# Kernel tuning notes

Hardware: AMD Instinct MI355X
Metric: run time of the kernel (lower is better)

## Reference

```python
import jax, jax.numpy as jnp
import numpy as np

B, T, C_IN, H, W = 128, 12, 10, 25, 25
HID = 64
DN = ('NCHW', 'OIHW', 'NCHW')


def setup_inputs() -> dict:
    key = jax.random.key(0)
    ks = jax.random.split(key, 8)
    x = jax.random.normal(ks[0], (B, T, C_IN, H, W), dtype=jnp.float32)
    # ConvLSTM cell: conv over concat([x, h]) -> 4*HID gate channels, 3x3 kernel
    conv_w = jax.random.normal(ks[1], (4 * HID, C_IN + HID, 3, 3), dtype=jnp.float32) * 0.05
    conv_b = jnp.zeros((4 * HID,), dtype=jnp.float32)
    # MLP head: hidden*25*25 -> 16 -> 8 -> 2
    w1 = jax.random.normal(ks[2], (HID * H * W, 16), dtype=jnp.float32) * 0.01
    b1 = jnp.zeros((16,), dtype=jnp.float32)
    w2 = jax.random.normal(ks[3], (16, 8), dtype=jnp.float32) * 0.1
    b2 = jnp.zeros((8,), dtype=jnp.float32)
    w3 = jax.random.normal(ks[4], (8, 2), dtype=jnp.float32) * 0.1
    b3 = jnp.zeros((2,), dtype=jnp.float32)
    return {"x": x, "conv_w": conv_w, "conv_b": conv_b,
            "w1": w1, "b1": b1, "w2": w2, "b2": b2, "w3": w3, "b3": b3}


def _convlstm_last_h(x, conv_w, conv_b):
    # x: (B,T,C,H,W); returns last hidden state h_T: (B,HID,H,W)
    h0 = jnp.zeros((x.shape[0], HID, H, W), dtype=x.dtype)
    c0 = jnp.zeros_like(h0)

    def step(carry, xt):
        h, c = carry
        inp = jnp.concatenate([xt, h], axis=1)              # (B, C+HID, H, W)
        gates = jax.lax.conv_general_dilated(
            inp, conv_w, window_strides=(1, 1), padding='SAME',
            dimension_numbers=DN) + conv_b[None, :, None, None]  # (B,4*HID,H,W)
        i, f, o, g = jnp.split(gates, 4, axis=1)
        i, f, o = jax.nn.sigmoid(i), jax.nn.sigmoid(f), jax.nn.sigmoid(o)
        g = jnp.tanh(g)
        c_new = f * c + i * g
        h_new = o * jnp.tanh(c_new)
        return (h_new, c_new), None

    (h_last, _), _ = jax.lax.scan(step, (h0, c0), jnp.swapaxes(x, 0, 1))
    return h_last


def reference(x, conv_w, conv_b, w1, b1, w2, b2, w3, b3):
    h = _convlstm_last_h(x, conv_w, conv_b)          # (B,HID,25,25)
    h = jax.nn.relu(h).reshape(h.shape[0], -1)       # flatten
    # dropout is identity in eval mode
    h = jax.nn.relu(h @ w1 + b1)
    h = jax.nn.relu(h @ w2 + b2)
    logits = h @ w3 + b3                             # (B,2)
    return jax.nn.log_softmax(logits, axis=1)
```

## Files before the change

kernel.cpp:

```cpp
#include <hip/hip_runtime.h>
#include <hip/hip_bf16.h>
#include <math.h>

#define BATCH 128
#define TT    12
#define CIN   10
#define HID   64
#define PLANE 625
#define NU    10
#define IPB   50000
#define NKB   45
#define CSZ   (BATCH*PLANE*HID)
#define KSPLIT 10

typedef __attribute__((ext_vector_type(8)))  short bf16x8;
typedef __attribute__((ext_vector_type(16))) float f32x16;

__device__ __forceinline__ float fsigm(float v){ return 1.f/(1.f+__expf(-v)); }
__device__ __forceinline__ float ftanh(float v){ return 1.f - 2.f/(__expf(2.f*v)+1.f); }
__device__ __forceinline__ unsigned short f2bf(float v){
    __hip_bfloat16 b = __float2bfloat16(v);
    return *reinterpret_cast<unsigned short*>(&b);
}

__global__ void k_wprep(const float* __restrict__ w, unsigned short* __restrict__ wpk){
    int tid = blockIdx.x*256 + threadIdx.x;
    if (tid >= NKB*8*64) return;
    int lane = tid & 63;
    int nt   = (tid >> 6) & 7;
    int kb   = tid >> 9;
    int tap = kb/5, ci = kb - tap*5;
    int ky = tap/3, kx = tap - ky*3;
    int g = lane & 3, jlo = (lane & 31) >> 2, kh = lane >> 5;
    int o = g*64 + nt*8 + jlo;
    union { unsigned short u[8]; float4 f; } pk;
    #pragma unroll
    for (int e = 0; e < 8; ++e){
        int ch = ci*16 + kh*8 + e;
        float v = (ch < 74) ? w[((o*74 + ch)*3 + ky)*3 + kx] : 0.f;
        pk.u[e] = f2bf(v);
    }
    *reinterpret_cast<float4*>(wpk + (size_t)tid*8) = pk.f;
}

__global__ void k_w1prep(const float* __restrict__ w1, float* __restrict__ w1t){
    int tid = blockIdx.x*256 + threadIdx.x;
    if (tid >= 40000*4) return;
    int rowp = tid >> 2, f4 = tid & 3;
    int m = rowp >> 6, j = rowp & 63;
    const float4* src = (const float4*)(w1 + (size_t)(j*625 + m)*16);
    ((float4*)(w1t + (size_t)rowp*16))[f4] = src[f4];
}

__global__ void k_xcopy(const float* __restrict__ x, unsigned short* __restrict__ inp, int t){
    int idx = blockIdx.x*256 + threadIdx.x;
    if (idx >= BATCH*CIN*PLANE) return;
    int m  = idx % PLANE;
    int r  = idx / PLANE;
    int ch = r % CIN;
    int b  = r / CIN;
    float v = x[((size_t)(b*TT + t)*CIN + ch)*PLANE + m];
    inp[(size_t)b*IPB + ((((ch>>3)*PLANE) + m)<<3) + (ch&7)] = f2bf(v);
}

__global__ __launch_bounds__(512) void k_gemm(
    const float* __restrict__ x,
    const unsigned short* __restrict__ inp,
    unsigned short* __restrict__ inpn,
    const unsigned short* __restrict__ wpk,
    const float* __restrict__ bias,
    float* __restrict__ cbuf,
    unsigned short* __restrict__ hbf,
    int t)
{
    __shared__ __align__(16) unsigned short at2[1620*8];

    const int tid  = threadIdx.x;
    const int mg   = blockIdx.x;
    const int b    = blockIdx.y;
    const int lane = tid & 63;
    const int nt   = tid >> 6;
    const int rlo  = (mg*64)/25;

    const unsigned short* ib = inp + (size_t)b*IPB;
    for (int idx = tid; idx < 1620; idx += 512){
        int q   = idx/162, pix = idx - q*162;
        int rr  = pix/27,  cc  = pix - rr*27;
        int gr  = rlo - 1 + rr, gc = cc - 1;
        float4 v = {0.f,0.f,0.f,0.f};
        if ((unsigned)gr < 25u && (unsigned)gc < 25u)
            v = *reinterpret_cast<const float4*>(ib + (((size_t)q*PLANE + gr*25 + gc)<<3));
        *reinterpret_cast<float4*>(at2 + ((size_t)idx<<3)) = v;
    }

    const int kh = lane >> 5;
    const unsigned short* ap[2];
    #pragma unroll
    for (int mt = 0; mt < 2; ++mt){
        int m = mg*64 + mt*32 + (lane & 31);
        int row = m/25, col = m - row*25;
        int pm = (row - rlo + 1)*27 + col;
        ap[mt] = at2 + kh*1296 + ((pm - 27) << 3);
    }

    f32x16 acc[2];
    #pragma unroll
    for (int mt = 0; mt < 2; ++mt)
        #pragma unroll
        for (int e = 0; e < 16; ++e) acc[mt][e] = 0.f;

    __syncthreads();

    const bf16x8* wptr = reinterpret_cast<const bf16x8*>(wpk) + nt*64 + lane;
    bf16x8 bcur = *wptr;
    const unsigned short *a0 = ap[0], *a1 = ap[1];
    #pragma unroll 1
    for (int tap = 0; tap < 9; ++tap){
        #pragma unroll
        for (int ci = 0; ci < 5; ++ci){
            bf16x8 bnxt = wptr[512];
            wptr += 512;
            bf16x8 f0 = *reinterpret_cast<const bf16x8*>(a0 + ci*2592);
            bf16x8 f1 = *reinterpret_cast<const bf16x8*>(a1 + ci*2592);
            acc[0] = __builtin_amdgcn_mfma_f32_32x32x16_bf16(f0, bcur, acc[0], 0,0,0);
            acc[1] = __builtin_amdgcn_mfma_f32_32x32x16_bf16(f1, bcur, acc[1], 0,0,0);
            bcur = bnxt;
        }
        const int d = (tap == 2 || tap == 5) ? 25*8 : 8;
        a0 += d; a1 += d;
    }

    const int g   = lane & 3;
    const int jlo = (lane & 31) >> 2;
    const int j   = nt*8 + jlo;
    const float bown = bias[g*64 + j];
    const float sA = (g == 3) ? 2.f : 1.f;
    const float sB = (g == 3) ? -1.f : 0.f;
    const int  mbase = mg*64 + 4*kh;
    const bool gb0 = (g & 1), gb1 = (g & 2);
    float* cb = cbuf + (size_t)b*PLANE*HID;
    unsigned short* hn  = inpn + (size_t)b*IPB;
    unsigned short* hfb = hbf  + (size_t)b*40000;
    const int chh = CIN + j, uh = chh >> 3, sh = chh & 7;

    #pragma unroll
    for (int mt = 0; mt < 2; ++mt){
        #pragma unroll
        for (int rq = 0; rq < 4; ++rq){
            float v0 = fmaf(sA, fsigm(sA*(acc[mt][rq*4+0] + bown)), sB);
            float v1 = fmaf(sA, fsigm(sA*(acc[mt][rq*4+1] + bown)), sB);
            float v2 = fmaf(sA, fsigm(sA*(acc[mt][rq*4+2] + bown)), sB);
            float v3 = fmaf(sA, fsigm(sA*(acc[mt][rq*4+3] + bown)), sB);
            float s;
            s = __shfl_xor(gb0 ? v0 : v1, 1); if (gb0) v0 = s; else v1 = s;
            s = __shfl_xor(gb0 ? v2 : v3, 1); if (gb0) v2 = s; else v3 = s;
            s = __shfl_xor(gb1 ? v0 : v2, 2); if (gb1) v0 = s; else v2 = s;
            s = __shfl_xor(gb1 ? v1 : v3, 2); if (gb1) v1 = s; else v3 = s;
            const int m = mbase + mt*32 + g + 8*rq;
            if (m < PLANE){
                float co = cb[m*HID + j];
                float cn = fmaf(v1, co, v0*v3);
                float h  = v2 * ftanh(cn);
                if (t < TT-1){
                    cb[m*HID + j] = cn;
                    hn[((uh*PLANE + m) << 3) + sh] = f2bf(h);
                } else {
                    hfb[m*64 + j] = f2bf(h > 0.f ? h : 0.f);
                }
            }
        }
    }

    if (t < TT-1){
        const float* xn = x + (size_t)(b*TT + t + 1)*CIN*PLANE;
        for (int idx = tid; idx < 640; idx += 512){
            int ch = idx >> 6, mi = idx & 63;
            int m = mg*64 + mi;
            if (m < PLANE)
                inpn[(size_t)b*IPB + ((((ch>>3)*PLANE) + m)<<3) + (ch&7)] =
                    f2bf(xn[ch*PLANE + m]);
        }
    }
}

__global__ __launch_bounds__(256) void k_mlp1(
    const unsigned short* __restrict__ hbf, const float* __restrict__ w1t,
    float* __restrict__ part)
{
    __shared__ float xw[4][4][16];
    const int ks = blockIdx.x, bg = blockIdx.y, tid = threadIdx.x;
    const int kw0 = ks*4000, kw1 = kw0 + 4000;
    const unsigned short* h0 = hbf + (size_t)(bg*4+0)*40000;
    const unsigned short* h1 = hbf + (size_t)(bg*4+1)*40000;
    const unsigned short* h2 = hbf + (size_t)(bg*4+2)*40000;
    const unsigned short* h3 = hbf + (size_t)(bg*4+3)*40000;

    float acc[4][16];
    #pragma unroll
    for (int bi = 0; bi < 4; ++bi)
        #pragma unroll
        for (int n = 0; n < 16; ++n) acc[bi][n] = 0.f;

    for (int kw = kw0 + tid*2; kw < kw1; kw += 512){
        const float4* wp = (const float4*)(w1t + (size_t)kw*16);
        float4 q0 = wp[0], q1 = wp[1], q2 = wp[2], q3 = wp[3];
        float4 r0 = wp[4], r1 = wp[5], r2 = wp[6], r3 = wp[7];
        unsigned int u0 = *(const unsigned int*)(h0 + kw);
        unsigned int u1 = *(const unsigned int*)(h1 + kw);
        unsigned int u2 = *(const unsigned int*)(h2 + kw);
        unsigned int u3 = *(const unsigned int*)(h3 + kw);
        #define ACC1(bi, u) { \
            float fl = __uint_as_float((u) << 16); \
            float fh = __uint_as_float((u) & 0xffff0000u); \
            acc[bi][ 0]=fmaf(fl,q0.x,fmaf(fh,r0.x,acc[bi][ 0])); \
            acc[bi][ 1]=fmaf(fl,q0.y,fmaf(fh,r0.y,acc[bi][ 1])); \
            acc[bi][ 2]=fmaf(fl,q0.z,fmaf(fh,r0.z,acc[bi][ 2])); \
            acc[bi][ 3]=fmaf(fl,q0.w,fmaf(fh,r0.w,acc[bi][ 3])); \
            acc[bi][ 4]=fmaf(fl,q1.x,fmaf(fh,r1.x,acc[bi][ 4])); \
            acc[bi][ 5]=fmaf(fl,q1.y,fmaf(fh,r1.y,acc[bi][ 5])); \
            acc[bi][ 6]=fmaf(fl,q1.z,fmaf(fh,r1.z,acc[bi][ 6])); \
            acc[bi][ 7]=fmaf(fl,q1.w,fmaf(fh,r1.w,acc[bi][ 7])); \
            acc[bi][ 8]=fmaf(fl,q2.x,fmaf(fh,r2.x,acc[bi][ 8])); \
            acc[bi][ 9]=fmaf(fl,q2.y,fmaf(fh,r2.y,acc[bi][ 9])); \
            acc[bi][10]=fmaf(fl,q2.z,fmaf(fh,r2.z,acc[bi][10])); \
            acc[bi][11]=fmaf(fl,q2.w,fmaf(fh,r2.w,acc[bi][11])); \
            acc[bi][12]=fmaf(fl,q3.x,fmaf(fh,r3.x,acc[bi][12])); \
            acc[bi][13]=fmaf(fl,q3.y,fmaf(fh,r3.y,acc[bi][13])); \
            acc[bi][14]=fmaf(fl,q3.z,fmaf(fh,r3.z,acc[bi][14])); \
            acc[bi][15]=fmaf(fl,q3.w,fmaf(fh,r3.w,acc[bi][15])); }
        ACC1(0, u0) ACC1(1, u1) ACC1(2, u2) ACC1(3, u3)
        #undef ACC1
    }

    #pragma unroll
    for (int d = 1; d < 64; d <<= 1)
        #pragma unroll
        for (int bi = 0; bi < 4; ++bi)
            #pragma unroll
            for (int n = 0; n < 16; ++n) acc[bi][n] += __shfl_xor(acc[bi][n], d);
    if ((tid & 63) == 0){
        int w = tid >> 6;
        #pragma unroll
        for (int bi = 0; bi < 4; ++bi)
            #pragma unroll
            for (int n = 0; n < 16; ++n) xw[w][bi][n] = acc[bi][n];
    }
    __syncthreads();
    if (tid < 64){
        int bi = tid >> 4, n = tid & 15;
        float s = xw[0][bi][n] + xw[1][bi][n] + xw[2][bi][n] + xw[3][bi][n];
        part[((size_t)(bg*4 + bi)*KSPLIT + ks)*16 + n] = s;
    }
}

__global__ __launch_bounds__(128) void k_mlp2(
    const float* __restrict__ part,
    const float* __restrict__ b1,
    const float* __restrict__ w2, const float* __restrict__ b2,
    const float* __restrict__ w3, const float* __restrict__ b3,
    float* __restrict__ out)
{
    const int b = threadIdx.x;
    float h1[16];
    #pragma unroll
    for (int i = 0; i < 16; ++i) h1[i] = b1[i];
    for (int s = 0; s < KSPLIT; ++s)
        #pragma unroll
        for (int i = 0; i < 16; ++i) h1[i] += part[((size_t)b * KSPLIT + s) * 16 + i];
    #pragma unroll
    for (int i = 0; i < 16; ++i) h1[i] = h1[i] > 0.f ? h1[i] : 0.f;

    float h2[8];
    #pragma unroll
    for (int i = 0; i < 8; ++i){
        float s2 = b2[i];
        #pragma unroll
        for (int k2 = 0; k2 < 16; ++k2) s2 += h1[k2] * w2[k2*8 + i];
        h2[i] = s2 > 0.f ? s2 : 0.f;
    }
    float l0 = b3[0], l1 = b3[1];
    #pragma unroll
    for (int k3 = 0; k3 < 8; ++k3){ l0 += h2[k3]*w3[k3*2]; l1 += h2[k3]*w3[k3*2+1]; }
    float m   = fmaxf(l0, l1);
    float lse = m + logf(__expf(l0 - m) + __expf(l1 - m));
    out[b*2 + 0] = l0 - lse;
    out[b*2 + 1] = l1 - lse;
}

extern "C" void kernel_launch(void* const* d_in, const int* in_sizes, int n_in,
                              void* d_out, int out_size, void* d_ws, size_t ws_size,
                              hipStream_t stream) {
    const float* x      = (const float*)d_in[0];
    const float* conv_w = (const float*)d_in[1];
    const float* conv_b = (const float*)d_in[2];
    const float* w1     = (const float*)d_in[3];
    const float* b1     = (const float*)d_in[4];
    const float* w2     = (const float*)d_in[5];
    const float* b2     = (const float*)d_in[6];
    const float* w3     = (const float*)d_in[7];
    const float* b3     = (const float*)d_in[8];
    float* out = (float*)d_out;

    unsigned short* inp0 = (unsigned short*)d_ws;
    unsigned short* inp1 = inp0 + (size_t)BATCH*IPB;
    float* c   = (float*)(inp1 + (size_t)BATCH*IPB);
    unsigned short* hbf = (unsigned short*)(c + CSZ);
    unsigned short* wpk = hbf + (size_t)BATCH*40000;
    float* w1t  = (float*)(wpk + (size_t)(NKB+1)*8*64*8);
    float* part = w1t + 640000;

    hipMemsetAsync(inp0, 0, (size_t)BATCH*IPB*2, stream);
    hipMemsetAsync(inp1, 0, (size_t)BATCH*IPB*2, stream);
    hipMemsetAsync(c,    0, (size_t)CSZ*4,       stream);

    k_wprep <<<dim3(90),   dim3(256), 0, stream>>>(conv_w, wpk);
    k_w1prep<<<dim3(625),  dim3(256), 0, stream>>>(w1, w1t);
    k_xcopy <<<dim3(3125), dim3(256), 0, stream>>>(x, inp0, 0);

    for (int t = 0; t < TT; ++t){
        unsigned short* ic  = (t & 1) ? inp1 : inp0;
        unsigned short* in_ = (t & 1) ? inp0 : inp1;
        k_gemm<<<dim3(10, BATCH), dim3(512), 0, stream>>>(x, ic, in_, wpk, conv_b, c, hbf, t);
    }
    k_mlp1<<<dim3(KSPLIT, 32), dim3(256), 0, stream>>>(hbf, w1t, part);
    k_mlp2<<<dim3(1), dim3(128), 0, stream>>>(part, b1, w2, b2, w3, b3, out);
}
```

Measured before the change: 625.0 us.

## Double M tile per block and stage conv weights into LDS via async loads

Result: slower. 711.4 us (+13.8%).

```diff
diff --git a/kernel.cpp b/kernel.cpp
--- a/kernel.cpp
+++ b/kernel.cpp
@@ -10,6 +10,7 @@
 #define NU    10
 #define IPB   50000
 #define NKB   45
+#define NKB_ALLOC (NKB+6)
 #define CSZ   (BATCH*PLANE*HID)
 #define KSPLIT 10
 
@@ -63,6 +64,9 @@
     inp[(size_t)b*IPB + ((((ch>>3)*PLANE) + m)<<3) + (ch&7)] = f2bf(v);
 }
 
+__device__ constexpr int TOFF[9] = {0,8,16,216,224,232,432,440,448};
+#define AOFF(kb) (TOFF[(kb)/5] + ((kb)%5)*3456)
+
 __global__ __launch_bounds__(512) void k_gemm(
     const float* __restrict__ x,
     const unsigned short* __restrict__ inp,
@@ -73,20 +77,23 @@
     unsigned short* __restrict__ hbf,
     int t)
 {
-    __shared__ __align__(16) unsigned short at2[1620*8];
+    __shared__ __align__(16) unsigned short at2[2160*8];
+    __shared__ __align__(16) unsigned short wls[2][8192];
 
     const int tid  = threadIdx.x;
     const int mg   = blockIdx.x;
     const int b    = blockIdx.y;
     const int lane = tid & 63;
-    const int nt   = tid >> 6;
-    const int rlo  = (mg*64)/25;
+    const int w    = tid >> 6;
+    const int ntp  = w & 3;
+    const int mtp  = w >> 2;
+    const int r0row = (mg*128)/25;
 
     const unsigned short* ib = inp + (size_t)b*IPB;
-    for (int idx = tid; idx < 1620; idx += 512){
-        int q   = idx/162, pix = idx - q*162;
+    for (int idx = tid; idx < 2160; idx += 512){
+        int q   = idx/216, pix = idx - q*216;
         int rr  = pix/27,  cc  = pix - rr*27;
-        int gr  = rlo - 1 + rr, gc = cc - 1;
+        int gr  = r0row - 1 + rr, gc = cc - 1;
         float4 v = {0.f,0.f,0.f,0.f};
         if ((unsigned)gr < 25u && (unsigned)gc < 25u)
             v = *reinterpret_cast<const float4*>(ib + (((size_t)q*PLANE + gr*25 + gc)<<3));
@@ -94,78 +101,101 @@
     }
 
     const int kh = lane >> 5;
-    const unsigned short* ap[2];
-    #pragma unroll
-    for (int mt = 0; mt < 2; ++mt){
-        int m = mg*64 + mt*32 + (lane & 31);
-        int row = m/25, col = m - row*25;
-        int pm = (row - rlo + 1)*27 + col;
-        ap[mt] = at2 + kh*1296 + ((pm - 27) << 3);
-    }
-
-    f32x16 acc[2];
-    #pragma unroll
-    for (int mt = 0; mt < 2; ++mt)
-        #pragma unroll
-        for (int e = 0; e < 16; ++e) acc[mt][e] = 0.f;
-
-    __syncthreads();
-
-    const bf16x8* wptr = reinterpret_cast<const bf16x8*>(wpk) + nt*64 + lane;
-    bf16x8 bcur = *wptr;
-    const unsigned short *a0 = ap[0], *a1 = ap[1];
-    #pragma unroll 1
-    for (int tap = 0; tap < 9; ++tap){
-        #pragma unroll
-        for (int ci = 0; ci < 5; ++ci){
-            bf16x8 bnxt = wptr[512];
-            wptr += 512;
-            bf16x8 f0 = *reinterpret_cast<const bf16x8*>(a0 + ci*2592);
-            bf16x8 f1 = *reinterpret_cast<const bf16x8*>(a1 + ci*2592);
-            acc[0] = __builtin_amdgcn_mfma_f32_32x32x16_bf16(f0, bcur, acc[0], 0,0,0);
-            acc[1] = __builtin_amdgcn_mfma_f32_32x32x16_bf16(f1, bcur, acc[1], 0,0,0);
-            bcur = bnxt;
+    const unsigned short *a0, *a1;
+    {
+        int m0 = mg*128 + (mtp*2+0)*32 + (lane & 31);
+        int r_ = m0/25, c_ = m0 - r_*25;
+        a0 = at2 + kh*1728 + (((r_ - r0row + 1)*27 + c_ - 27) << 3);
+        int m1 = mg*128 + (mtp*2+1)*32 + (lane & 31);
+        r_ = m1/25; c_ = m1 - r_*25;
+        a1 = at2 + kh*1728 + (((r_ - r0row + 1)*27 + c_ - 27) << 3);
+    }
+    const unsigned short* bb = &wls[0][0] + ntp*1024 + lane*8;
+
+    auto stageB = [&](int kb, int bufsel, int slot){
+        __builtin_amdgcn_global_load_lds(
+            (const __attribute__((address_space(1))) void*)(wpk + ((size_t)(kb*8 + w))*512 + lane*8),
+            (__attribute__((address_space(3))) void*)(&wls[bufsel][slot*4096 + w*512]),
+            16, 0, 0);
+    };
+
+    f32x16 acc00, acc01, acc10, acc11;
+    #pragma unroll
+    for (int e = 0; e < 16; ++e){ acc00[e]=0.f; acc01[e]=0.f; acc10[e]=0.f; acc11[e]=0.f; }
+
+    stageB(0, 0, 0);
+    stageB(1, 0, 1);
+
+    #define KBSTEP(kb, buf, q) { \
+        bf16x8 b0 = *reinterpret_cast<const bf16x8*>(bb + (buf)*8192 + (q)*4096); \
+        bf16x8 b1 = *reinterpret_cast<const bf16x8*>(bb + (buf)*8192 + (q)*4096 + 512); \
+        bf16x8 f0 = *reinterpret_cast<const bf16x8*>(a0 + AOFF(kb)); \
+        bf16x8 f1 = *reinterpret_cast<const bf16x8*>(a1 + AOFF(kb)); \
+        acc00 = __builtin_amdgcn_mfma_f32_32x32x16_bf16(f0, b0, acc00, 0,0,0); \
+        acc10 = __builtin_amdgcn_mfma_f32_32x32x16_bf16(f1, b0, acc10, 0,0,0); \
+        acc01 = __builtin_amdgcn_mfma_f32_32x32x16_bf16(f0, b1, acc01, 0,0,0); \
+        acc11 = __builtin_amdgcn_mfma_f32_32x32x16_bf16(f1, b1, acc11, 0,0,0); \
+    }
+
+    #pragma unroll
+    for (int p = 0; p < 23; ++p){
+        __syncthreads();
+        if (p < 21){
+            stageB(2*p+2, (p+1)&1, 0);
+            stageB(2*p+3, (p+1)&1, 1);
+        } else if (p == 21){
+            stageB(44, 0, 0);
         }
-        const int d = (tap == 2 || tap == 5) ? 25*8 : 8;
-        a0 += d; a1 += d;
-    }
+        KBSTEP(2*p, p&1, 0);
+        if (2*p+1 < NKB) KBSTEP(2*p+1, p&1, 1);
+    }
+    #undef KBSTEP
 
     const int g   = lane & 3;
     const int jlo = (lane & 31) >> 2;
-    const int j   = nt*8 + jlo;
-    const float bown = bias[g*64 + j];
+    const int j0  = (ntp*2+0)*8 + jlo;
+    const int j1  = (ntp*2+1)*8 + jlo;
+    const float bown0 = bias[g*64 + j0];
+    const float bown1 = bias[g*64 + j1];
     const float sA = (g == 3) ? 2.f : 1.f;
     const float sB = (g == 3) ? -1.f : 0.f;
-    const int  mbase = mg*64 + 4*kh;
+    const int  mbase = mg*128 + mtp*64 + 4*kh;
     const bool gb0 = (g & 1), gb1 = (g & 2);
     float* cb = cbuf + (size_t)b*PLANE*HID;
     unsigned short* hn  = inpn + (size_t)b*IPB;
     unsigned short* hfb = hbf  + (size_t)b*40000;
-    const int chh = CIN + j, uh = chh >> 3, sh = chh & 7;
-
-    #pragma unroll
-    for (int mt = 0; mt < 2; ++mt){
-        #pragma unroll
-        for (int rq = 0; rq < 4; ++rq){
-            float v0 = fmaf(sA, fsigm(sA*(acc[mt][rq*4+0] + bown)), sB);
-            float v1 = fmaf(sA, fsigm(sA*(acc[mt][rq*4+1] + bown)), sB);
-            float v2 = fmaf(sA, fsigm(sA*(acc[mt][rq*4+2] + bown)), sB);
-            float v3 = fmaf(sA, fsigm(sA*(acc[mt][rq*4+3] + bown)), sB);
-            float s;
-            s = __shfl_xor(gb0 ? v0 : v1, 1); if (gb0) v0 = s; else v1 = s;
-            s = __shfl_xor(gb0 ? v2 : v3, 1); if (gb0) v2 = s; else v3 = s;
-            s = __shfl_xor(gb1 ? v0 : v2, 2); if (gb1) v0 = s; else v2 = s;
-            s = __shfl_xor(gb1 ? v1 : v3, 2); if (gb1) v1 = s; else v3 = s;
-            const int m = mbase + mt*32 + g + 8*rq;
-            if (m < PLANE){
-                float co = cb[m*HID + j];
-                float cn = fmaf(v1, co, v0*v3);
-                float h  = v2 * ftanh(cn);
-                if (t < TT-1){
-                    cb[m*HID + j] = cn;
-                    hn[((uh*PLANE + m) << 3) + sh] = f2bf(h);
-                } else {
-                    hfb[m*64 + j] = f2bf(h > 0.f ? h : 0.f);
+
+    #pragma unroll
+    for (int mt_ = 0; mt_ < 2; ++mt_){
+        #pragma unroll
+        for (int n = 0; n < 2; ++n){
+            const f32x16& A = (mt_ == 0) ? (n == 0 ? acc00 : acc01)
+                                         : (n == 0 ? acc10 : acc11);
+            const int   jj = n ? j1 : j0;
+            const float bw = n ? bown1 : bown0;
+            const int  chh = CIN + jj, uh = chh >> 3, sh = chh & 7;
+            #pragma unroll
+            for (int rq = 0; rq < 4; ++rq){
+                float v0 = fmaf(sA, fsigm(sA*(A[rq*4+0] + bw)), sB);
+                float v1 = fmaf(sA, fsigm(sA*(A[rq*4+1] + bw)), sB);
+                float v2 = fmaf(sA, fsigm(sA*(A[rq*4+2] + bw)), sB);
+                float v3 = fmaf(sA, fsigm(sA*(A[rq*4+3] + bw)), sB);
+                float s;
+                s = __shfl_xor(gb0 ? v0 : v1, 1); if (gb0) v0 = s; else v1 = s;
+                s = __shfl_xor(gb0 ? v2 : v3, 1); if (gb0) v2 = s; else v3 = s;
+                s = __shfl_xor(gb1 ? v0 : v2, 2); if (gb1) v0 = s; else v2 = s;
+                s = __shfl_xor(gb1 ? v1 : v3, 2); if (gb1) v1 = s; else v3 = s;
+                const int m = mbase + mt_*32 + g + 8*rq;
+                if (m < PLANE){
+                    float co = cb[m*HID + jj];
+                    float cn = fmaf(v1, co, v0*v3);
+                    float h  = v2 * ftanh(cn);
+                    if (t < TT-1){
+                        cb[m*HID + jj] = cn;
+                        hn[((uh*PLANE + m) << 3) + sh] = f2bf(h);
+                    } else {
+                        hfb[m*64 + jj] = f2bf(h > 0.f ? h : 0.f);
+                    }
                 }
             }
         }
@@ -173,9 +203,9 @@
 
     if (t < TT-1){
         const float* xn = x + (size_t)(b*TT + t + 1)*CIN*PLANE;
-        for (int idx = tid; idx < 640; idx += 512){
-            int ch = idx >> 6, mi = idx & 63;
-            int m = mg*64 + mi;
+        for (int idx = tid; idx < 1280; idx += 512){
+            int ch = idx >> 7, mi = idx & 127;
+            int m = mg*128 + mi;
             if (m < PLANE)
                 inpn[(size_t)b*IPB + ((((ch>>3)*PLANE) + m)<<3) + (ch&7)] =
                     f2bf(xn[ch*PLANE + m]);
@@ -306,7 +336,7 @@
     float* c   = (float*)(inp1 + (size_t)BATCH*IPB);
     unsigned short* hbf = (unsigned short*)(c + CSZ);
     unsigned short* wpk = hbf + (size_t)BATCH*40000;
-    float* w1t  = (float*)(wpk + (size_t)(NKB+1)*8*64*8);
+    float* w1t  = (float*)(wpk + (size_t)NKB_ALLOC*8*64*8);
     float* part = w1t + 640000;
 
     hipMemsetAsync(inp0, 0, (size_t)BATCH*IPB*2, stream);
@@ -320,7 +350,7 @@
     for (int t = 0; t < TT; ++t){
         unsigned short* ic  = (t & 1) ? inp1 : inp0;
         unsigned short* in_ = (t & 1) ? inp0 : inp1;
-        k_gemm<<<dim3(10, BATCH), dim3(512), 0, stream>>>(x, ic, in_, wpk, conv_b, c, hbf, t);
+        k_gemm<<<dim3(5, BATCH), dim3(512), 0, stream>>>(x, ic, in_, wpk, conv_b, c, hbf, t);
     }
     k_mlp1<<<dim3(KSPLIT, 32), dim3(256), 0, stream>>>(hbf, w1t, part);
     k_mlp2<<<dim3(1), dim3(128), 0, stream>>>(part, b1, w2, b2, w3, b3, out);
```

## Enlarge conv GEMM register tile to 128 pixels by 2 gate tiles per wave

Applied to the files above, without the earlier changes.

After: 1.184 ms. 89.5% more time.

```diff
diff --git a/kernel.cpp b/kernel.cpp
--- a/kernel.cpp
+++ b/kernel.cpp
@@ -10,6 +10,7 @@
 #define NU    10
 #define IPB   50000
 #define NKB   45
+#define NKB_ALLOC (NKB+6)
 #define CSZ   (BATCH*PLANE*HID)
 #define KSPLIT 10
 
@@ -63,7 +64,7 @@
     inp[(size_t)b*IPB + ((((ch>>3)*PLANE) + m)<<3) + (ch&7)] = f2bf(v);
 }
 
-__global__ __launch_bounds__(512) void k_gemm(
+__global__ __launch_bounds__(256) void k_gemm(
     const float* __restrict__ x,
     const unsigned short* __restrict__ inp,
     unsigned short* __restrict__ inpn,
@@ -73,20 +74,21 @@
     unsigned short* __restrict__ hbf,
     int t)
 {
-    __shared__ __align__(16) unsigned short at2[1620*8];
+    __shared__ __align__(16) unsigned short at2[2160*8];
 
     const int tid  = threadIdx.x;
     const int mg   = blockIdx.x;
     const int b    = blockIdx.y;
     const int lane = tid & 63;
-    const int nt   = tid >> 6;
-    const int rlo  = (mg*64)/25;
+    const int ntp  = tid >> 6;
+    const int nt0  = ntp*2;
+    const int r0row = (mg*128)/25;
 
     const unsigned short* ib = inp + (size_t)b*IPB;
-    for (int idx = tid; idx < 1620; idx += 512){
-        int q   = idx/162, pix = idx - q*162;
+    for (int idx = tid; idx < 2160; idx += 256){
+        int q   = idx/216, pix = idx - q*216;
         int rr  = pix/27,  cc  = pix - rr*27;
-        int gr  = rlo - 1 + rr, gc = cc - 1;
+        int gr  = r0row - 1 + rr, gc = cc - 1;
         float4 v = {0.f,0.f,0.f,0.f};
         if ((unsigned)gr < 25u && (unsigned)gc < 25u)
             v = *reinterpret_cast<const float4*>(ib + (((size_t)q*PLANE + gr*25 + gc)<<3));
@@ -94,78 +96,108 @@
     }
 
     const int kh = lane >> 5;
-    const unsigned short* ap[2];
-    #pragma unroll
-    for (int mt = 0; mt < 2; ++mt){
-        int m = mg*64 + mt*32 + (lane & 31);
-        int row = m/25, col = m - row*25;
-        int pm = (row - rlo + 1)*27 + col;
-        ap[mt] = at2 + kh*1296 + ((pm - 27) << 3);
-    }
-
-    f32x16 acc[2];
-    #pragma unroll
-    for (int mt = 0; mt < 2; ++mt)
-        #pragma unroll
-        for (int e = 0; e < 16; ++e) acc[mt][e] = 0.f;
+    const unsigned short *p0, *p1, *p2, *p3;
+    {
+        int m0 = mg*128 + 0*32 + (lane & 31), r_ = m0/25, c_ = m0 - r_*25;
+        p0 = at2 + kh*1728 + (((r_ - r0row + 1)*27 + c_ - 27) << 3);
+        int m1 = mg*128 + 1*32 + (lane & 31); r_ = m1/25; c_ = m1 - r_*25;
+        p1 = at2 + kh*1728 + (((r_ - r0row + 1)*27 + c_ - 27) << 3);
+        int m2 = mg*128 + 2*32 + (lane & 31); r_ = m2/25; c_ = m2 - r_*25;
+        p2 = at2 + kh*1728 + (((r_ - r0row + 1)*27 + c_ - 27) << 3);
+        int m3 = mg*128 + 3*32 + (lane & 31); r_ = m3/25; c_ = m3 - r_*25;
+        p3 = at2 + kh*1728 + (((r_ - r0row + 1)*27 + c_ - 27) << 3);
+    }
+
+    f32x16 acc[4][2];
+    #pragma unroll
+    for (int mt = 0; mt < 4; ++mt)
+        #pragma unroll
+        for (int n = 0; n < 2; ++n)
+            #pragma unroll
+            for (int e = 0; e < 16; ++e) acc[mt][n][e] = 0.f;
 
     __syncthreads();
 
-    const bf16x8* wptr = reinterpret_cast<const bf16x8*>(wpk) + nt*64 + lane;
-    bf16x8 bcur = *wptr;
-    const unsigned short *a0 = ap[0], *a1 = ap[1];
+    const bf16x8* wf = reinterpret_cast<const bf16x8*>(wpk) + nt0*64 + lane;
+    bf16x8 Bc0 = wf[0], Bc1 = wf[64];
+    bf16x8 fc0 = *reinterpret_cast<const bf16x8*>(p0);
+    bf16x8 fc1 = *reinterpret_cast<const bf16x8*>(p1);
+    bf16x8 fc2 = *reinterpret_cast<const bf16x8*>(p2);
+    bf16x8 fc3 = *reinterpret_cast<const bf16x8*>(p3);
+
     #pragma unroll 1
     for (int tap = 0; tap < 9; ++tap){
+        const int d = (tap == 2 || tap == 5) ? 25*8 : 8;
+        const unsigned short* q0 = (tap < 8) ? p0 + d : p0;
+        const unsigned short* q1 = (tap < 8) ? p1 + d : p1;
+        const unsigned short* q2 = (tap < 8) ? p2 + d : p2;
+        const unsigned short* q3 = (tap < 8) ? p3 + d : p3;
+        const bf16x8* wnx = wf + 2560;
+
         #pragma unroll
         for (int ci = 0; ci < 5; ++ci){
-            bf16x8 bnxt = wptr[512];
-            wptr += 512;
-            bf16x8 f0 = *reinterpret_cast<const bf16x8*>(a0 + ci*2592);
-            bf16x8 f1 = *reinterpret_cast<const bf16x8*>(a1 + ci*2592);
-            acc[0] = __builtin_amdgcn_mfma_f32_32x32x16_bf16(f0, bcur, acc[0], 0,0,0);
-            acc[1] = __builtin_amdgcn_mfma_f32_32x32x16_bf16(f1, bcur, acc[1], 0,0,0);
-            bcur = bnxt;
+            bf16x8 nB0 = (ci < 4) ? wf[(ci+1)*512]      : wnx[0];
+            bf16x8 nB1 = (ci < 4) ? wf[(ci+1)*512 + 64] : wnx[64];
+            bf16x8 t0 = *reinterpret_cast<const bf16x8*>((ci < 4) ? p0 + (ci+1)*3456 : q0);
+            bf16x8 t1 = *reinterpret_cast<const bf16x8*>((ci < 4) ? p1 + (ci+1)*3456 : q1);
+            bf16x8 t2 = *reinterpret_cast<const bf16x8*>((ci < 4) ? p2 + (ci+1)*3456 : q2);
+            bf16x8 t3 = *reinterpret_cast<const bf16x8*>((ci < 4) ? p3 + (ci+1)*3456 : q3);
+            acc[0][0] = __builtin_amdgcn_mfma_f32_32x32x16_bf16(fc0, Bc0, acc[0][0], 0,0,0);
+            acc[0][1] = __builtin_amdgcn_mfma_f32_32x32x16_bf16(fc0, Bc1, acc[0][1], 0,0,0);
+            acc[1][0] = __builtin_amdgcn_mfma_f32_32x32x16_bf16(fc1, Bc0, acc[1][0], 0,0,0);
+            acc[1][1] = __builtin_amdgcn_mfma_f32_32x32x16_bf16(fc1, Bc1, acc[1][1], 0,0,0);
+            acc[2][0] = __builtin_amdgcn_mfma_f32_32x32x16_bf16(fc2, Bc0, acc[2][0], 0,0,0);
+            acc[2][1] = __builtin_amdgcn_mfma_f32_32x32x16_bf16(fc2, Bc1, acc[2][1], 0,0,0);
+            acc[3][0] = __builtin_amdgcn_mfma_f32_32x32x16_bf16(fc3, Bc0, acc[3][0], 0,0,0);
+            acc[3][1] = __builtin_amdgcn_mfma_f32_32x32x16_bf16(fc3, Bc1, acc[3][1], 0,0,0);
+            Bc0 = nB0; Bc1 = nB1; fc0 = t0; fc1 = t1; fc2 = t2; fc3 = t3;
         }
-        const int d = (tap == 2 || tap == 5) ? 25*8 : 8;
-        a0 += d; a1 += d;
+        wf = wnx; p0 = q0; p1 = q1; p2 = q2; p3 = q3;
     }
 
     const int g   = lane & 3;
     const int jlo = (lane & 31) >> 2;
-    const int j   = nt*8 + jlo;
-    const float bown = bias[g*64 + j];
+    const int j0  = (nt0+0)*8 + jlo;
+    const int j1  = (nt0+1)*8 + jlo;
+    const float bown0 = bias[g*64 + j0];
+    const float bown1 = bias[g*64 + j1];
     const float sA = (g == 3) ? 2.f : 1.f;
     const float sB = (g == 3) ? -1.f : 0.f;
-    const int  mbase = mg*64 + 4*kh;
+    const int  mbase = mg*128 + 4*kh;
     const bool gb0 = (g & 1), gb1 = (g & 2);
     float* cb = cbuf + (size_t)b*PLANE*HID;
     unsigned short* hn  = inpn + (size_t)b*IPB;
     unsigned short* hfb = hbf  + (size_t)b*40000;
-    const int chh = CIN + j, uh = chh >> 3, sh = chh & 7;
-
-    #pragma unroll
-    for (int mt = 0; mt < 2; ++mt){
-        #pragma unroll
-        for (int rq = 0; rq < 4; ++rq){
-            float v0 = fmaf(sA, fsigm(sA*(acc[mt][rq*4+0] + bown)), sB);
-            float v1 = fmaf(sA, fsigm(sA*(acc[mt][rq*4+1] + bown)), sB);
-            float v2 = fmaf(sA, fsigm(sA*(acc[mt][rq*4+2] + bown)), sB);
-            float v3 = fmaf(sA, fsigm(sA*(acc[mt][rq*4+3] + bown)), sB);
-            float s;
-            s = __shfl_xor(gb0 ? v0 : v1, 1); if (gb0) v0 = s; else v1 = s;
-            s = __shfl_xor(gb0 ? v2 : v3, 1); if (gb0) v2 = s; else v3 = s;
-            s = __shfl_xor(gb1 ? v0 : v2, 2); if (gb1) v0 = s; else v2 = s;
-            s = __shfl_xor(gb1 ? v1 : v3, 2); if (gb1) v1 = s; else v3 = s;
-            const int m = mbase + mt*32 + g + 8*rq;
-            if (m < PLANE){
-                float co = cb[m*HID + j];
-                float cn = fmaf(v1, co, v0*v3);
-                float h  = v2 * ftanh(cn);
-                if (t < TT-1){
-                    cb[m*HID + j] = cn;
-                    hn[((uh*PLANE + m) << 3) + sh] = f2bf(h);
-                } else {
-                    hfb[m*64 + j] = f2bf(h > 0.f ? h : 0.f);
+
+    #pragma unroll
+    for (int mt = 0; mt < 4; ++mt){
+        #pragma unroll
+        for (int n = 0; n < 2; ++n){
+            const int   jj = n ? j1 : j0;
+            const float bw = n ? bown1 : bown0;
+            const int  chh = CIN + jj, uh = chh >> 3, sh = chh & 7;
+            #pragma unroll
+            for (int rq = 0; rq < 4; ++rq){
+                float v0 = fmaf(sA, fsigm(sA*(acc[mt][n][rq*4+0] + bw)), sB);
+                float v1 = fmaf(sA, fsigm(sA*(acc[mt][n][rq*4+1] + bw)), sB);
+                float v2 = fmaf(sA, fsigm(sA*(acc[mt][n][rq*4+2] + bw)), sB);
+                float v3 = fmaf(sA, fsigm(sA*(acc[mt][n][rq*4+3] + bw)), sB);
+                float s;
+                s = __shfl_xor(gb0 ? v0 : v1, 1); if (gb0) v0 = s; else v1 = s;
+                s = __shfl_xor(gb0 ? v2 : v3, 1); if (gb0) v2 = s; else v3 = s;
+                s = __shfl_xor(gb1 ? v0 : v2, 2); if (gb1) v0 = s; else v2 = s;
+                s = __shfl_xor(gb1 ? v1 : v3, 2); if (gb1) v1 = s; else v3 = s;
+                const int m = mbase + mt*32 + g + 8*rq;
+                if (m < PLANE){
+                    float co = cb[m*HID + jj];
+                    float cn = fmaf(v1, co, v0*v3);
+                    float h  = v2 * ftanh(cn);
+                    if (t < TT-1){
+                        cb[m*HID + jj] = cn;
+                        hn[((uh*PLANE + m) << 3) + sh] = f2bf(h);
+                    } else {
+                        hfb[m*64 + jj] = f2bf(h > 0.f ? h : 0.f);
+                    }
                 }
             }
         }
@@ -173,9 +205,9 @@
 
     if (t < TT-1){
         const float* xn = x + (size_t)(b*TT + t + 1)*CIN*PLANE;
-        for (int idx = tid; idx < 640; idx += 512){
-            int ch = idx >> 6, mi = idx & 63;
-            int m = mg*64 + mi;
+        for (int idx = tid; idx < 1280; idx += 256){
+            int ch = idx >> 7, mi = idx & 127;
+            int m = mg*128 + mi;
             if (m < PLANE)
                 inpn[(size_t)b*IPB + ((((ch>>3)*PLANE) + m)<<3) + (ch&7)] =
                     f2bf(xn[ch*PLANE + m]);
@@ -306,7 +338,7 @@
     float* c   = (float*)(inp1 + (size_t)BATCH*IPB);
     unsigned short* hbf = (unsigned short*)(c + CSZ);
     unsigned short* wpk = hbf + (size_t)BATCH*40000;
-    float* w1t  = (float*)(wpk + (size_t)(NKB+1)*8*64*8);
+    float* w1t  = (float*)(wpk + (size_t)NKB_ALLOC*8*64*8);
     float* part = w1t + 640000;
 
     hipMemsetAsync(inp0, 0, (size_t)BATCH*IPB*2, stream);
@@ -320,7 +352,7 @@
     for (int t = 0; t < TT; ++t){
         unsigned short* ic  = (t & 1) ? inp1 : inp0;
         unsigned short* in_ = (t & 1) ? inp0 : inp1;
-        k_gemm<<<dim3(10, BATCH), dim3(512), 0, stream>>>(x, ic, in_, wpk, conv_b, c, hbf, t);
+        k_gemm<<<dim3(5, BATCH), dim3(256), 0, stream>>>(x, ic, in_, wpk, conv_b, c, hbf, t);
     }
     k_mlp1<<<dim3(KSPLIT, 32), dim3(256), 0, stream>>>(hbf, w1t, part);
     k_mlp2<<<dim3(1), dim3(128), 0, stream>>>(part, b1, w2, b2, w3, b3, out);
```

## Fuse all timesteps into one persistent conv kernel with inter-block flag sync

Applied to the files above, without the earlier changes.

Result: slower. 2.404 ms (+284.6%).

```diff
diff --git a/kernel.cpp b/kernel.cpp
--- a/kernel.cpp
+++ b/kernel.cpp
@@ -7,11 +7,14 @@
 #define CIN   10
 #define HID   64
 #define PLANE 625
-#define NU    10
 #define IPB   50000
 #define NKB   45
+#define NKB_ALLOC (NKB+6)
 #define CSZ   (BATCH*PLANE*HID)
 #define KSPLIT 10
+#define NPIX  405
+#define USTR  (NPIX*8)
+#define CISTR (2*NPIX*8)
 
 typedef __attribute__((ext_vector_type(8)))  short bf16x8;
 typedef __attribute__((ext_vector_type(16))) float f32x16;
@@ -63,122 +66,169 @@
     inp[(size_t)b*IPB + ((((ch>>3)*PLANE) + m)<<3) + (ch&7)] = f2bf(v);
 }
 
-__global__ __launch_bounds__(512) void k_gemm(
+__global__ __launch_bounds__(512, 2) void k_conv(
     const float* __restrict__ x,
-    const unsigned short* __restrict__ inp,
-    unsigned short* __restrict__ inpn,
+    unsigned short* __restrict__ inp0,
+    unsigned short* __restrict__ inp1,
     const unsigned short* __restrict__ wpk,
     const float* __restrict__ bias,
     float* __restrict__ cbuf,
     unsigned short* __restrict__ hbf,
-    int t)
+    int* __restrict__ flags)
 {
-    __shared__ __align__(16) unsigned short at2[1620*8];
+    __shared__ __align__(16) unsigned short at2[10*NPIX*8];
 
     const int tid  = threadIdx.x;
-    const int mg   = blockIdx.x;
+    const int half = blockIdx.x;
     const int b    = blockIdx.y;
     const int lane = tid & 63;
-    const int nt   = tid >> 6;
-    const int rlo  = (mg*64)/25;
-
-    const unsigned short* ib = inp + (size_t)b*IPB;
-    for (int idx = tid; idx < 1620; idx += 512){
-        int q   = idx/162, pix = idx - q*162;
-        int rr  = pix/27,  cc  = pix - rr*27;
-        int gr  = rlo - 1 + rr, gc = cc - 1;
-        float4 v = {0.f,0.f,0.f,0.f};
-        if ((unsigned)gr < 25u && (unsigned)gc < 25u)
-            v = *reinterpret_cast<const float4*>(ib + (((size_t)q*PLANE + gr*25 + gc)<<3));
-        *reinterpret_cast<float4*>(at2 + ((size_t)idx<<3)) = v;
-    }
-
-    const int kh = lane >> 5;
-    const unsigned short* ap[2];
-    #pragma unroll
-    for (int mt = 0; mt < 2; ++mt){
-        int m = mg*64 + mt*32 + (lane & 31);
-        int row = m/25, col = m - row*25;
-        int pm = (row - rlo + 1)*27 + col;
-        ap[mt] = at2 + kh*1296 + ((pm - 27) << 3);
-    }
-
-    f32x16 acc[2];
-    #pragma unroll
-    for (int mt = 0; mt < 2; ++mt)
-        #pragma unroll
-        for (int e = 0; e < 16; ++e) acc[mt][e] = 0.f;
-
-    __syncthreads();
-
-    const bf16x8* wptr = reinterpret_cast<const bf16x8*>(wpk) + nt*64 + lane;
-    bf16x8 bcur = *wptr;
-    const unsigned short *a0 = ap[0], *a1 = ap[1];
-    #pragma unroll 1
-    for (int tap = 0; tap < 9; ++tap){
-        #pragma unroll
-        for (int ci = 0; ci < 5; ++ci){
-            bf16x8 bnxt = wptr[512];
-            wptr += 512;
-            bf16x8 f0 = *reinterpret_cast<const bf16x8*>(a0 + ci*2592);
-            bf16x8 f1 = *reinterpret_cast<const bf16x8*>(a1 + ci*2592);
-            acc[0] = __builtin_amdgcn_mfma_f32_32x32x16_bf16(f0, bcur, acc[0], 0,0,0);
-            acc[1] = __builtin_amdgcn_mfma_f32_32x32x16_bf16(f1, bcur, acc[1], 0,0,0);
-            bcur = bnxt;
-        }
-        const int d = (tap == 2 || tap == 5) ? 25*8 : 8;
-        a0 += d; a1 += d;
+    const int w    = tid >> 6;
+    const int ntp  = w & 3;
+    const int mh   = w >> 2;
+    const int gr0  = half ? 12 : -1;
+    const int mb0  = half ? 325 : 0;
+    const int kh   = lane >> 5;
+
+    const unsigned short* ab[6];
+    int mtbase[6];
+    #pragma unroll
+    for (int q = 0; q < 6; ++q){
+        int base = mb0 + (mh*6 + q)*32;
+        mtbase[q] = base;
+        int m0 = base + (lane & 31);
+        if (m0 > 624) m0 = 624;
+        int row = m0/25, col = m0 - row*25;
+        ab[q] = at2 + kh*USTR + (((row - 1 - gr0)*27 + col) << 3);
     }
 
     const int g   = lane & 3;
     const int jlo = (lane & 31) >> 2;
-    const int j   = nt*8 + jlo;
-    const float bown = bias[g*64 + j];
+    const int j0  = (ntp*2+0)*8 + jlo;
+    const int j1  = (ntp*2+1)*8 + jlo;
+    const float bown0 = bias[g*64 + j0];
+    const float bown1 = bias[g*64 + j1];
     const float sA = (g == 3) ? 2.f : 1.f;
     const float sB = (g == 3) ? -1.f : 0.f;
-    const int  mbase = mg*64 + 4*kh;
     const bool gb0 = (g & 1), gb1 = (g & 2);
     float* cb = cbuf + (size_t)b*PLANE*HID;
-    unsigned short* hn  = inpn + (size_t)b*IPB;
-    unsigned short* hfb = hbf  + (size_t)b*40000;
-    const int chh = CIN + j, uh = chh >> 3, sh = chh & 7;
-
-    #pragma unroll
-    for (int mt = 0; mt < 2; ++mt){
-        #pragma unroll
-        for (int rq = 0; rq < 4; ++rq){
-            float v0 = fmaf(sA, fsigm(sA*(acc[mt][rq*4+0] + bown)), sB);
-            float v1 = fmaf(sA, fsigm(sA*(acc[mt][rq*4+1] + bown)), sB);
-            float v2 = fmaf(sA, fsigm(sA*(acc[mt][rq*4+2] + bown)), sB);
-            float v3 = fmaf(sA, fsigm(sA*(acc[mt][rq*4+3] + bown)), sB);
-            float s;
-            s = __shfl_xor(gb0 ? v0 : v1, 1); if (gb0) v0 = s; else v1 = s;
-            s = __shfl_xor(gb0 ? v2 : v3, 1); if (gb0) v2 = s; else v3 = s;
-            s = __shfl_xor(gb1 ? v0 : v2, 2); if (gb1) v0 = s; else v2 = s;
-            s = __shfl_xor(gb1 ? v1 : v3, 2); if (gb1) v1 = s; else v3 = s;
-            const int m = mbase + mt*32 + g + 8*rq;
-            if (m < PLANE){
-                float co = cb[m*HID + j];
-                float cn = fmaf(v1, co, v0*v3);
-                float h  = v2 * ftanh(cn);
-                if (t < TT-1){
-                    cb[m*HID + j] = cn;
-                    hn[((uh*PLANE + m) << 3) + sh] = f2bf(h);
-                } else {
-                    hfb[m*64 + j] = f2bf(h > 0.f ? h : 0.f);
+    unsigned short* hfb = hbf + (size_t)b*40000;
+    const int chh0 = CIN + j0, uh0 = chh0 >> 3, sh0 = chh0 & 7;
+    const int chh1 = CIN + j1, uh1 = chh1 >> 3, sh1 = chh1 & 7;
+    const int mcount = half ? 300 : 325;
+    int* const fown  = flags + (b*2 + half)*16;
+    int* const fothr = flags + (b*2 + (half^1))*16;
+
+    for (int t = 0; t < TT; ++t){
+        const unsigned short* ic  = (t & 1) ? inp1 : inp0;
+        unsigned short*       in_ = (t & 1) ? inp0 : inp1;
+        const unsigned short* ib  = ic  + (size_t)b*IPB;
+        unsigned short*       hn  = in_ + (size_t)b*IPB;
+
+        for (int idx = tid; idx < 10*NPIX; idx += 512){
+            int u   = idx/NPIX, pix = idx - u*NPIX;
+            int rr  = pix/27,   cc  = pix - rr*27;
+            int gr  = gr0 + rr, gc = cc - 1;
+            float4 v = {0.f,0.f,0.f,0.f};
+            if ((unsigned)gr < 25u && (unsigned)gc < 25u)
+                v = *reinterpret_cast<const float4*>(ib + (((size_t)u*PLANE + gr*25 + gc)<<3));
+            *reinterpret_cast<float4*>(at2 + ((size_t)idx<<3)) = v;
+        }
+
+        f32x16 acc[6][2];
+        #pragma unroll
+        for (int q = 0; q < 6; ++q)
+            #pragma unroll
+            for (int n = 0; n < 2; ++n)
+                #pragma unroll
+                for (int e = 0; e < 16; ++e) acc[q][n][e] = 0.f;
+
+        __syncthreads();
+
+        const bf16x8* wtap = reinterpret_cast<const bf16x8*>(wpk) + (ntp*2)*64 + lane;
+        const unsigned short *a0 = ab[0], *a1 = ab[1], *a2 = ab[2],
+                             *a3 = ab[3], *a4 = ab[4], *a5 = ab[5];
+        #pragma unroll 1
+        for (int tap = 0; tap < 9; ++tap){
+            #pragma unroll
+            for (int ci = 0; ci < 5; ++ci){
+                bf16x8 B0 = wtap[ci*512];
+                bf16x8 B1 = wtap[ci*512 + 64];
+                bf16x8 f0 = *reinterpret_cast<const bf16x8*>(a0 + ci*CISTR);
+                bf16x8 f1 = *reinterpret_cast<const bf16x8*>(a1 + ci*CISTR);
+                bf16x8 f2 = *reinterpret_cast<const bf16x8*>(a2 + ci*CISTR);
+                bf16x8 f3 = *reinterpret_cast<const bf16x8*>(a3 + ci*CISTR);
+                bf16x8 f4 = *reinterpret_cast<const bf16x8*>(a4 + ci*CISTR);
+                bf16x8 f5 = *reinterpret_cast<const bf16x8*>(a5 + ci*CISTR);
+                acc[0][0] = __builtin_amdgcn_mfma_f32_32x32x16_bf16(f0, B0, acc[0][0], 0,0,0);
+                acc[0][1] = __builtin_amdgcn_mfma_f32_32x32x16_bf16(f0, B1, acc[0][1], 0,0,0);
+                acc[1][0] = __builtin_amdgcn_mfma_f32_32x32x16_bf16(f1, B0, acc[1][0], 0,0,0);
+                acc[1][1] = __builtin_amdgcn_mfma_f32_32x32x16_bf16(f1, B1, acc[1][1], 0,0,0);
+                acc[2][0] = __builtin_amdgcn_mfma_f32_32x32x16_bf16(f2, B0, acc[2][0], 0,0,0);
+                acc[2][1] = __builtin_amdgcn_mfma_f32_32x32x16_bf16(f2, B1, acc[2][1], 0,0,0);
+                acc[3][0] = __builtin_amdgcn_mfma_f32_32x32x16_bf16(f3, B0, acc[3][0], 0,0,0);
+                acc[3][1] = __builtin_amdgcn_mfma_f32_32x32x16_bf16(f3, B1, acc[3][1], 0,0,0);
+                acc[4][0] = __builtin_amdgcn_mfma_f32_32x32x16_bf16(f4, B0, acc[4][0], 0,0,0);
+                acc[4][1] = __builtin_amdgcn_mfma_f32_32x32x16_bf16(f4, B1, acc[4][1], 0,0,0);
+                acc[5][0] = __builtin_amdgcn_mfma_f32_32x32x16_bf16(f5, B0, acc[5][0], 0,0,0);
+                acc[5][1] = __builtin_amdgcn_mfma_f32_32x32x16_bf16(f5, B1, acc[5][1], 0,0,0);
+            }
+            const int d = (tap == 2 || tap == 5) ? 25*8 : 8;
+            a0 += d; a1 += d; a2 += d; a3 += d; a4 += d; a5 += d;
+            wtap += 2560;
+        }
+
+        #pragma unroll
+        for (int q = 0; q < 6; ++q){
+            #pragma unroll
+            for (int n = 0; n < 2; ++n){
+                const int   jj = n ? j1 : j0;
+                const float bw = n ? bown1 : bown0;
+                const int   uh = n ? uh1 : uh0;
+                const int   sh = n ? sh1 : sh0;
+                #pragma unroll
+                for (int rq = 0; rq < 4; ++rq){
+                    float v0 = fmaf(sA, fsigm(sA*(acc[q][n][rq*4+0] + bw)), sB);
+                    float v1 = fmaf(sA, fsigm(sA*(acc[q][n][rq*4+1] + bw)), sB);
+                    float v2 = fmaf(sA, fsigm(sA*(acc[q][n][rq*4+2] + bw)), sB);
+                    float v3 = fmaf(sA, fsigm(sA*(acc[q][n][rq*4+3] + bw)), sB);
+                    float s;
+                    s = __shfl_xor(gb0 ? v0 : v1, 1); if (gb0) v0 = s; else v1 = s;
+                    s = __shfl_xor(gb0 ? v2 : v3, 1); if (gb0) v2 = s; else v3 = s;
+                    s = __shfl_xor(gb1 ? v0 : v2, 2); if (gb1) v0 = s; else v2 = s;
+                    s = __shfl_xor(gb1 ? v1 : v3, 2); if (gb1) v1 = s; else v3 = s;
+                    const int m = mtbase[q] + 4*kh + g + 8*rq;
+                    if (m < PLANE){
+                        float co = cb[m*HID + jj];
+                        float cn = fmaf(v1, co, v0*v3);
+                        float h  = v2 * ftanh(cn);
+                        if (t < TT-1){
+                            cb[m*HID + jj] = cn;
+                            hn[((uh*PLANE + m) << 3) + sh] = f2bf(h);
+                        } else {
+                            hfb[m*64 + jj] = f2bf(h > 0.f ? h : 0.f);
+                        }
+                    }
                 }
             }
         }
-    }
-
-    if (t < TT-1){
-        const float* xn = x + (size_t)(b*TT + t + 1)*CIN*PLANE;
-        for (int idx = tid; idx < 640; idx += 512){
-            int ch = idx >> 6, mi = idx & 63;
-            int m = mg*64 + mi;
-            if (m < PLANE)
-                inpn[(size_t)b*IPB + ((((ch>>3)*PLANE) + m)<<3) + (ch&7)] =
-                    f2bf(xn[ch*PLANE + m]);
+
+        if (t < TT-1){
+            const float* xn = x + (size_t)(b*TT + t + 1)*CIN*PLANE;
+            #pragma unroll 1
+            for (int ch = 0; ch < CIN; ++ch){
+                for (int mi = tid; mi < mcount; mi += 512){
+                    int m = mb0 + mi;
+                    hn[(((ch>>3)*PLANE + m)<<3) + (ch&7)] = f2bf(xn[ch*PLANE + m]);
+                }
+            }
+            __threadfence();
+            __syncthreads();
+            if (tid == 0){
+                atomicExch(&fown[t], 1);
+                while (atomicAdd(&fothr[t], 0) == 0) __builtin_amdgcn_s_sleep(8);
+            }
+            __syncthreads();
+            __threadfence();
         }
     }
 }
@@ -306,22 +356,22 @@
     float* c   = (float*)(inp1 + (size_t)BATCH*IPB);
     unsigned short* hbf = (unsigned short*)(c + CSZ);
     unsigned short* wpk = hbf + (size_t)BATCH*40000;
-    float* w1t  = (float*)(wpk + (size_t)(NKB+1)*8*64*8);
+    float* w1t  = (float*)(wpk + (size_t)NKB_ALLOC*8*64*8);
     float* part = w1t + 640000;
-
-    hipMemsetAsync(inp0, 0, (size_t)BATCH*IPB*2, stream);
-    hipMemsetAsync(inp1, 0, (size_t)BATCH*IPB*2, stream);
-    hipMemsetAsync(c,    0, (size_t)CSZ*4,       stream);
+    int*   flags = (int*)(part + BATCH*KSPLIT*16);
+
+    hipMemsetAsync(inp0,  0, (size_t)BATCH*IPB*2, stream);
+    hipMemsetAsync(inp1,  0, (size_t)BATCH*IPB*2, stream);
+    hipMemsetAsync(c,     0, (size_t)CSZ*4,       stream);
+    hipMemsetAsync(flags, 0, (size_t)BATCH*2*16*4, stream);
 
     k_wprep <<<dim3(90),   dim3(256), 0, stream>>>(conv_w, wpk);
     k_w1prep<<<dim3(625),  dim3(256), 0, stream>>>(w1, w1t);
     k_xcopy <<<dim3(3125), dim3(256), 0, stream>>>(x, inp0, 0);
 
-    for (int t = 0; t < TT; ++t){
-        unsigned short* ic  = (t & 1) ? inp1 : inp0;
-        unsigned short* in_ = (t & 1) ? inp0 : inp1;
-        k_gemm<<<dim3(10, BATCH), dim3(512), 0, stream>>>(x, ic, in_, wpk, conv_b, c, hbf, t);
-    }
+    k_conv<<<dim3(2, BATCH), dim3(512), 0, stream>>>(x, inp0, inp1, wpk, conv_b,
+                                                     c, hbf, flags);
+
     k_mlp1<<<dim3(KSPLIT, 32), dim3(256), 0, stream>>>(hbf, w1t, part);
     k_mlp2<<<dim3(1), dim3(128), 0, stream>>>(part, b1, w2, b2, w3, b3, out);
 }
```
